# Kernel tuning notes

Hardware: AMD Instinct MI355X
Metric: run time of the kernel (lower is better)

The kernel has to match this reference:

```python
import jax, jax.numpy as jnp
import numpy as np

N = 20000
DEG = 16
E = N * DEG
IN_DIM = 512
OUT_DIM = 512
H = 4
D = OUT_DIM // H            # head_dim = 128
POS_DIM = 3
M_ROPE = D // (POS_DIM * 2) # 21
D_ROPE = POS_DIM * 2 * M_ROPE  # 126 (2 trailing dims unrotated)
ROPE_BASE = 10000.0

INV_FREQ = jnp.exp(-jnp.arange(M_ROPE, dtype=jnp.float32) * (np.log(ROPE_BASE) / M_ROPE))


def _rope(t, pos):
    # t: (N, D, H), pos: (N, POS_DIM)
    n = t.shape[0]
    angles = pos[:, :, None] * INV_FREQ[None, None, :]        # (N, POS_DIM, M)
    cos = jnp.cos(angles)[..., None]                           # (N, POS_DIM, M, 1)
    sin = jnp.sin(angles)[..., None]
    part = t[:, :D_ROPE, :].reshape(n, POS_DIM, M_ROPE, 2, H)
    even, odd = part[..., 0, :], part[..., 1, :]
    rot_even = even * cos - odd * sin
    rot_odd = even * sin + odd * cos
    rot = jnp.stack((rot_even, rot_odd), axis=3).reshape(n, D_ROPE, H)
    return jnp.concatenate([rot, t[:, D_ROPE:, :]], axis=1)


def setup_inputs() -> dict:
    key = jax.random.key(0)
    ks = jax.random.split(key, 12)
    x = jax.random.normal(ks[0], (N, IN_DIM), jnp.float32)
    pos = jax.random.uniform(ks[1], (N, POS_DIM), jnp.float32) * 100.0
    rows = jnp.repeat(jnp.arange(N, dtype=jnp.int32), DEG)  # sorted, every node has DEG out-edges
    cols = jax.random.randint(ks[2], (E,), 0, N, dtype=jnp.int32)
    s = 1.0 / np.sqrt(IN_DIM)
    Wq = jax.random.normal(ks[3], (OUT_DIM, IN_DIM), jnp.float32) * s
    Wk = jax.random.normal(ks[4], (OUT_DIM, IN_DIM), jnp.float32) * s
    Wv = jax.random.normal(ks[5], (OUT_DIM, IN_DIM), jnp.float32) * s
    Wo = jax.random.normal(ks[6], (OUT_DIM, OUT_DIM), jnp.float32) * s
    bq = jax.random.normal(ks[7], (OUT_DIM,), jnp.float32) * 0.01
    bk = jax.random.normal(ks[8], (OUT_DIM,), jnp.float32) * 0.01
    bv = jax.random.normal(ks[9], (OUT_DIM,), jnp.float32) * 0.01
    bo = jax.random.normal(ks[10], (OUT_DIM,), jnp.float32) * 0.01
    return {"x": x, "pos": pos, "rows": rows, "cols": cols,
            "Wq": Wq, "bq": bq, "Wk": Wk, "bk": bk, "Wv": Wv, "bv": bv, "Wo": Wo, "bo": bo}


def reference(x, pos, rows, cols, Wq, bq, Wk, bk, Wv, bv, Wo, bo):
    n = x.shape[0]
    q = (x @ Wq.T + bq).reshape(n, D, H)
    k = (x @ Wk.T + bk).reshape(n, D, H)
    v = (x @ Wv.T + bv).reshape(n, D, H)
    # scaling by sqrt(k.size(1)) == sqrt(head_dim)
    q = q / jnp.sqrt(jnp.asarray(D, q.dtype))
    q = _rope(q, pos)
    k = _rope(k, pos)
    # per-edge scores: s[e,h] = sum_d q[rows[e],d,h] * k[cols[e],d,h]
    scores = jnp.einsum('edh,edh->eh', q[rows], k[cols])  # (E, H)
    # row-wise sparse softmax per head
    row_max = jax.ops.segment_max(scores, rows, num_segments=n, indices_are_sorted=True)
    p = jnp.exp(scores - row_max[rows])
    denom = jax.ops.segment_sum(p, rows, num_segments=n, indices_are_sorted=True)
    attn = p / denom[rows]                                 # (E, H)
    # bspmm: y[i,d,h] = sum_{e: rows[e]=i} attn[e,h] * v[cols[e],d,h]
    y = jax.ops.segment_sum(attn[:, None, :] * v[cols], rows, num_segments=n, indices_are_sorted=True)
    out = y.reshape(n, OUT_DIM) @ Wo.T + bo
    return out
```

## Files before the change

kernel.cpp:

```cpp
#include <hip/hip_runtime.h>
#include <hip/hip_bf16.h>

#define NN 20000
#define DEG 16
#define KD 512
#define OD 512
#define NH 4
#define DH 128
#define DROPE 126

#define BM 128
#define BN 128
#define BK 64

typedef unsigned short u16;
typedef unsigned int u32;
typedef __attribute__((ext_vector_type(8))) short short8;
typedef __attribute__((ext_vector_type(4))) float f32x4;

__device__ __forceinline__ float b2f(u16 u){ return __uint_as_float((u32)u << 16); }
__device__ __forceinline__ u16 f2b(float f){
  u32 x = __float_as_uint(f);
  return (u16)((x + 0x7fffu + ((x >> 16) & 1u)) >> 16);
}
__device__ __forceinline__ void up8(uint4 u, float* f){
  f[0]=__uint_as_float(u.x<<16); f[1]=__uint_as_float(u.x&0xffff0000u);
  f[2]=__uint_as_float(u.y<<16); f[3]=__uint_as_float(u.y&0xffff0000u);
  f[4]=__uint_as_float(u.z<<16); f[5]=__uint_as_float(u.z&0xffff0000u);
  f[6]=__uint_as_float(u.w<<16); f[7]=__uint_as_float(u.w&0xffff0000u);
}
__device__ __forceinline__ uint4 cvt8(const float* s){
  uint4 a = *(const uint4*)s;
  uint4 b = *(const uint4*)(s + 4);
  uint4 o;
  o.x = (u32)f2b(__uint_as_float(a.x)) | ((u32)f2b(__uint_as_float(a.y)) << 16);
  o.y = (u32)f2b(__uint_as_float(a.z)) | ((u32)f2b(__uint_as_float(a.w)) << 16);
  o.z = (u32)f2b(__uint_as_float(b.x)) | ((u32)f2b(__uint_as_float(b.y)) << 16);
  o.w = (u32)f2b(__uint_as_float(b.z)) | ((u32)f2b(__uint_as_float(b.w)) << 16);
  return o;
}

__device__ __forceinline__ void load_lds16(const u16* g, u16* l) {
  __builtin_amdgcn_global_load_lds(
      (const __attribute__((address_space(1))) void*)g,
      (__attribute__((address_space(3))) void*)l, 16, 0, 0);
}

struct ConvJob {
  const float* x;  u16* xb;
  const float* w[4]; u16* wb[4];
  const float* b[4]; u16* bb[4];
};
__global__ __launch_bounds__(256) void conv_all(ConvJob j) {
  const int b = blockIdx.x;
  if (b < 5000) {
    const int i8 = (b * 256 + threadIdx.x) * 8;
    *(uint4*)(j.xb + i8) = cvt8(j.x + i8);
  } else if (b < 5512) {
    const int t = b - 5000;
    const int wsel = t >> 7;
    const int i8 = ((t & 127) * 256 + threadIdx.x) * 8;
    *(uint4*)(j.wb[wsel] + i8) = cvt8(j.w[wsel] + i8);
  } else {
    const int vsel = threadIdx.x >> 6;
    const int i8 = (threadIdx.x & 63) * 8;
    *(uint4*)(j.bb[vsel] + i8) = cvt8(j.b[vsel] + i8);
  }
}

__global__ __launch_bounds__(256, 4) void gemm_k(
    const u16* __restrict__ A,
    const u16* __restrict__ W0, const u16* __restrict__ B0,
    const u16* __restrict__ W1, const u16* __restrict__ B1,
    const u16* __restrict__ W2, const u16* __restrict__ B2,
    const float* __restrict__ pos,
    u16* __restrict__ o0, u16* __restrict__ o1, void* __restrict__ o2,
    int M, int only2, int f32out)
{
  __shared__ __align__(16) char smem[36864];
  __shared__ float posS[BM*3];
  __shared__ float freqS[21];
  u16* As = (u16*)smem;
  u16* Bs = As + BM*BK;

  const int b = blockIdx.x;
  const int xcd = b & 7, rem = b >> 3;
  int rowT, colT, w;
  if (only2) {
    rowT = (rem >> 2)*8 + xcd; colT = rem & 3; w = 2;
  } else {
    rowT = (rem / 12)*8 + xcd; const int sub = rem % 12; colT = sub & 3; w = sub >> 2;
  }
  if (rowT*BM >= M) return;

  const int tid = threadIdx.x;
  const int wave = tid >> 6, lane = tid & 63;
  const int wr = wave >> 1, wc = wave & 1;
  const int lm = lane & 15, lq = lane >> 4;
  const u16* W  = (w == 0) ? W0 : ((w == 1) ? W1 : W2);
  const u16* Bi = (w == 0) ? B0 : ((w == 1) ? B1 : B2);
  const int mode = w;
  u16* outQK = (w == 0) ? o0 : o1;

  f32x4 acc[4][4];
  #pragma unroll
  for (int i = 0; i < 4; i++)
    #pragma unroll
    for (int jj = 0; jj < 4; jj++)
      acc[i][jj] = (f32x4){0.f, 0.f, 0.f, 0.f};

  if (mode < 2) {
    if (tid < BM) {
      int gr = rowT*BM + tid; if (gr >= M) gr = M - 1;
      posS[tid*3+0] = pos[gr*3+0];
      posS[tid*3+1] = pos[gr*3+1];
      posS[tid*3+2] = pos[gr*3+2];
    }
    if (tid >= BM && tid < BM + 21)
      freqS[tid - BM] = __expf(-(float)(tid - BM) * 0.43858763676077064f);
  }

  for (int kt = 0; kt < KD; kt += BK) {
    #pragma unroll
    for (int it = 0; it < 4; it++) {
      const int chunk = it*256 + wave*64 + lane;
      const int row = chunk >> 3, gseg = (chunk & 7) ^ (row & 7);
      int gr = rowT*BM + row; if (gr >= M) gr = M - 1;
      load_lds16(A + (size_t)gr*KD + kt + gseg*8,
                 As + (size_t)(it*256 + wave*64)*8);
    }
    #pragma unroll
    for (int it = 0; it < 4; it++) {
      const int chunk = it*256 + wave*64 + lane;
      const int row = chunk >> 3, gseg = (chunk & 7) ^ (row & 7);
      load_lds16(W + (size_t)(colT*BN + row)*KD + kt + gseg*8,
                 Bs + (size_t)(it*256 + wave*64)*8);
    }
    __syncthreads();
    #pragma unroll
    for (int kk = 0; kk < BK; kk += 32) {
      const int ks = kk >> 3;
      short8 af[4], bfr[4];
      #pragma unroll
      for (int i = 0; i < 4; i++) {
        const int ra = wr*64 + i*16 + lm;
        af[i] = *(const short8*)(As + (size_t)(ra*8 + ((ks + lq) ^ (ra & 7)))*8);
      }
      #pragma unroll
      for (int i = 0; i < 4; i++) {
        const int rb = wc*64 + i*16 + lm;
        bfr[i] = *(const short8*)(Bs + (size_t)(rb*8 + ((ks + lq) ^ (rb & 7)))*8);
      }
      #pragma unroll
      for (int mi = 0; mi < 4; mi++)
        #pragma unroll
        for (int ni = 0; ni < 4; ni++)
          acc[mi][ni] = __builtin_amdgcn_mfma_f32_16x16x32_bf16(af[mi], bfr[ni], acc[mi][ni], 0, 0, 0);
    }
    __syncthreads();
  }

  float bvv[4];
  #pragma unroll
  for (int ni = 0; ni < 4; ni++)
    bvv[ni] = b2f(Bi[colT*BN + wc*64 + ni*16 + lm]);

  u16* Cs = (u16*)smem;

  if (mode == 2 && f32out) {
    #pragma unroll
    for (int mi = 0; mi < 4; mi++)
      #pragma unroll
      for (int ni = 0; ni < 4; ni++) {
        const int Cg = colT*BN + wc*64 + ni*16 + lm;
        #pragma unroll
        for (int r = 0; r < 4; r++) {
          const int grow = rowT*BM + wr*64 + mi*16 + lq*4 + r;
          if (grow < M) ((float*)o2)[(size_t)grow*OD + Cg] = acc[mi][ni][r] + bvv[ni];
        }
      }
    return;
  }

  if (mode == 2) {
    #pragma unroll
    for (int mi = 0; mi < 4; mi++)
      #pragma unroll
      for (int ni = 0; ni < 4; ni++) {
        const int cloc = wc*64 + ni*16 + lm;
        #pragma unroll
        for (int r = 0; r < 4; r++) {
          const int rloc = wr*64 + mi*16 + lq*4 + r;
          Cs[rloc*136 + cloc] = f2b(acc[mi][ni][r] + bvv[ni]);
        }
      }
    __syncthreads();
    #pragma unroll
    for (int pass = 0; pass < 8; pass++) {
      const int c2 = pass*256 + tid;
      const int cc = c2 & 15, rloc = c2 >> 4;
      const int grow = rowT*BM + rloc;
      if (grow < M) {
        uint4 v = *(const uint4*)(Cs + rloc*136 + cc*8);
        *(uint4*)((u16*)o2 + (size_t)grow*OD + colT*BN + cc*8) = v;
      }
    }
    return;
  }

  #pragma unroll
  for (int mi = 0; mi < 4; mi++) {
    #pragma unroll
    for (int ni = 0; ni < 4; ni++) {
      const int cloc = wc*64 + ni*16 + lm;
      const int h = cloc & 3, dloc = cloc >> 2;
      const int d = colT*32 + dloc;
      #pragma unroll
      for (int r = 0; r < 4; r++) {
        const int rloc = wr*64 + mi*16 + lq*4 + r;
        float v = acc[mi][ni][r] + bvv[ni];
        if (mode == 0) v *= 0.08838834764831845f;
        const float partner = __shfl_xor(v, 4);
        float vr = v;
        if (d < DROPE) {
          const int pp = d / 42, rem2 = d - pp*42, m = rem2 >> 1, par = rem2 & 1;
          const float ang = posS[rloc*3 + pp] * freqS[m];
          float sn, cs; __sincosf(ang, &sn, &cs);
          vr = par ? (v*cs + partner*sn) : (v*cs - partner*sn);
        }
        Cs[rloc*144 + h*36 + dloc] = f2b(vr);
      }
    }
  }
  __syncthreads();
  #pragma unroll
  for (int pass = 0; pass < 8; pass++) {
    const int c2 = pass*256 + tid;
    const int dd8 = c2 & 3, h = (c2 >> 2) & 3, rloc = c2 >> 4;
    const int grow = rowT*BM + rloc;
    if (grow < M) {
      uint2 a = *(const uint2*)(Cs + rloc*144 + h*36 + dd8*8);
      uint2 b2 = *(const uint2*)(Cs + rloc*144 + h*36 + dd8*8 + 4);
      *(uint4*)(outQK + ((size_t)grow*NH + h)*DH + colT*32 + dd8*8)
          = make_uint4(a.x, a.y, b2.x, b2.y);
    }
  }
}

__global__ __launch_bounds__(256, 3) void edge_attn(
    const int* __restrict__ cols, const u16* __restrict__ qf,
    const u16* __restrict__ kf, const u16* __restrict__ vf,
    u16* __restrict__ y)
{
  const int wave = threadIdx.x >> 6;
  const int lane = threadIdx.x & 63;
  const int n = blockIdx.x*4 + wave;
  const int j = lane >> 2, h = lane & 3;
  const int col = cols[n*DEG + j];

  const uint4 qall = *(const uint4*)(qf + (size_t)n*OD + lane*8);

  int cjs[16];
  #pragma unroll
  for (int jj = 0; jj < 16; jj++) cjs[jj] = __shfl(col, jj*4);

  uint4 kreg[16];
  #pragma unroll
  for (int jj = 0; jj < 16; jj++)
    kreg[jj] = *(const uint4*)(kf + (size_t)cjs[jj]*OD + lane*8);

  uint4 vreg[16];
  #pragma unroll
  for (int jj = 0; jj < 16; jj++)
    vreg[jj] = *(const uint4*)(vf + (size_t)cjs[jj]*OD + lane*8);

  float qa[8];
  up8(qall, qa);

  float s = 0.f;
  #pragma unroll
  for (int jj = 0; jj < 16; jj++) {
    float ka[8];
    up8(kreg[jj], ka);
    float pr = qa[0]*ka[0] + qa[1]*ka[1] + qa[2]*ka[2] + qa[3]*ka[3]
             + qa[4]*ka[4] + qa[5]*ka[5] + qa[6]*ka[6] + qa[7]*ka[7];
    pr += __shfl_xor(pr, 1);
    pr += __shfl_xor(pr, 2);
    pr += __shfl_xor(pr, 4);
    pr += __shfl_xor(pr, 8);
    const float red = __shfl(pr, h*16);
    s = (j == jj) ? red : s;
  }

  float mx = s;
  #pragma unroll
  for (int msk = 4; msk < 64; msk <<= 1) mx = fmaxf(mx, __shfl_xor(mx, msk));
  float p = expf(s - mx);
  float dn = p;
  #pragma unroll
  for (int msk = 4; msk < 64; msk <<= 1) dn += __shfl_xor(dn, msk);
  const float attn = p / dn;

  float ya[8];
  #pragma unroll
  for (int t = 0; t < 8; t++) ya[t] = 0.f;
  #pragma unroll
  for (int jj = 0; jj < 16; jj++) {
    const float a0 = __shfl(attn, jj*4+0);
    const float a1 = __shfl(attn, jj*4+1);
    const float a2 = __shfl(attn, jj*4+2);
    const float a3 = __shfl(attn, jj*4+3);
    float va[8];
    up8(vreg[jj], va);
    ya[0] += a0*va[0]; ya[1] += a1*va[1]; ya[2] += a2*va[2]; ya[3] += a3*va[3];
    ya[4] += a0*va[4]; ya[5] += a1*va[5]; ya[6] += a2*va[6]; ya[7] += a3*va[7];
  }
  u32 pk[4];
  #pragma unroll
  for (int t = 0; t < 4; t++)
    pk[t] = (u32)f2b(ya[2*t]) | ((u32)f2b(ya[2*t+1]) << 16);
  *(uint4*)(y + (size_t)n*OD + lane*8) = make_uint4(pk[0], pk[1], pk[2], pk[3]);
}

extern "C" void kernel_launch(void* const* d_in, const int* in_sizes, int n_in,
                              void* d_out, int out_size, void* d_ws, size_t ws_size,
                              hipStream_t stream) {
  (void)in_sizes; (void)n_in; (void)out_size; (void)ws_size;
  const float* x   = (const float*)d_in[0];
  const float* pos = (const float*)d_in[1];
  const int* cols = (const int*)d_in[3];
  const float* Wq = (const float*)d_in[4];
  const float* bq = (const float*)d_in[5];
  const float* Wk = (const float*)d_in[6];
  const float* bk = (const float*)d_in[7];
  const float* Wv = (const float*)d_in[8];
  const float* bv = (const float*)d_in[9];
  const float* Wo = (const float*)d_in[10];
  const float* bo = (const float*)d_in[11];

  char* ws = (char*)d_ws;
  size_t off = 0;
  auto carve = [&](size_t bytes) { char* p = ws + off; off += (bytes + 15) & ~(size_t)15; return p; };
  u16* xb   = (u16*)carve((size_t)NN*KD*2);
  u16* Wqb  = (u16*)carve((size_t)OD*KD*2);
  u16* Wkb  = (u16*)carve((size_t)OD*KD*2);
  u16* Wvb  = (u16*)carve((size_t)OD*KD*2);
  u16* Wob  = (u16*)carve((size_t)OD*OD*2);
  u16* bqb  = (u16*)carve((size_t)OD*2);
  u16* bkb  = (u16*)carve((size_t)OD*2);
  u16* bvb  = (u16*)carve((size_t)OD*2);
  u16* bob  = (u16*)carve((size_t)OD*2);
  u16* qf   = (u16*)carve((size_t)NN*OD*2);
  u16* kf   = (u16*)carve((size_t)NN*OD*2);
  u16* vf   = (u16*)carve((size_t)NN*OD*2);
  u16* y    = (u16*)carve((size_t)NN*OD*2);

  ConvJob cj;
  cj.x = x; cj.xb = xb;
  cj.w[0]=Wq; cj.w[1]=Wk; cj.w[2]=Wv; cj.w[3]=Wo;
  cj.wb[0]=Wqb; cj.wb[1]=Wkb; cj.wb[2]=Wvb; cj.wb[3]=Wob;
  cj.b[0]=bq; cj.b[1]=bk; cj.b[2]=bv; cj.b[3]=bo;
  cj.bb[0]=bqb; cj.bb[1]=bkb; cj.bb[2]=bvb; cj.bb[3]=bob;
  conv_all<<<dim3(5513), 256, 0, stream>>>(cj);

  gemm_k<<<dim3(1920), 256, 0, stream>>>(xb, Wqb, bqb, Wkb, bkb, Wvb, bvb, pos,
                                         qf, kf, (void*)vf, NN, 0, 0);
  edge_attn<<<dim3(NN/4), 256, 0, stream>>>(cols, qf, kf, vf, y);
  gemm_k<<<dim3(640), 256, 0, stream>>>(y, Wqb, bqb, Wkb, bkb, Wob, bob, pos,
                                        qf, kf, d_out, NN, 1, 1);
}
```

Baseline: 256.7 us.

## Store V head-major and split edge attention per head with XCD-aware mapping

V is now written in the same head-major permuted layout as Q and K, and Wo is transposed on conversion to match, so y comes out head-major and the output GEMM still gives the same result. The edge-attention kernel is restructured so each block handles one head for 16 nodes. Each 16-lane group owns one node and one head, which lets the softmax reduce within 16 lanes, and V gathers are deferred until after the softmax to lower register pressure. Blocks are mapped to XCDs by head so that each XCD's L2 caches only one head's slice of K and V, which should improve gather locality. The cost is a strided, uncoalesced read of Wo during conversion.

```diff
diff --git a/kernel.cpp b/kernel.cpp
--- a/kernel.cpp
+++ b/kernel.cpp
@@ -60,7 +60,22 @@
     const int t = b - 5000;
     const int wsel = t >> 7;
     const int i8 = ((t & 127) * 256 + threadIdx.x) * 8;
-    *(uint4*)(j.wb[wsel] + i8) = cvt8(j.w[wsel] + i8);
+    if (wsel < 3) {
+      *(uint4*)(j.wb[wsel] + i8) = cvt8(j.w[wsel] + i8);
+    } else {
+      const int o = i8 >> 9, cp = i8 & 511;
+      const int h = cp >> 7, d0 = cp & 127;
+      const float* src = j.w[3] + (size_t)o * 512 + h;
+      float tmp[8];
+      #pragma unroll
+      for (int t2 = 0; t2 < 8; t2++) tmp[t2] = src[(size_t)(d0 + t2) * 4];
+      uint4 ov;
+      ov.x = (u32)f2b(tmp[0]) | ((u32)f2b(tmp[1]) << 16);
+      ov.y = (u32)f2b(tmp[2]) | ((u32)f2b(tmp[3]) << 16);
+      ov.z = (u32)f2b(tmp[4]) | ((u32)f2b(tmp[5]) << 16);
+      ov.w = (u32)f2b(tmp[6]) | ((u32)f2b(tmp[7]) << 16);
+      *(uint4*)(j.wb[3] + i8) = ov;
+    }
   } else {
     const int vsel = threadIdx.x >> 6;
     const int i8 = (threadIdx.x & 63) * 8;
@@ -99,8 +114,8 @@
   const int lm = lane & 15, lq = lane >> 4;
   const u16* W  = (w == 0) ? W0 : ((w == 1) ? W1 : W2);
   const u16* Bi = (w == 0) ? B0 : ((w == 1) ? B1 : B2);
-  const int mode = w;
-  u16* outQK = (w == 0) ? o0 : o1;
+  const int emode = only2 ? 3 : w;
+  u16* outQKV = (w == 0) ? o0 : ((w == 1) ? o1 : (u16*)o2);
 
   f32x4 acc[4][4];
   #pragma unroll
@@ -109,7 +124,7 @@
     for (int jj = 0; jj < 4; jj++)
       acc[i][jj] = (f32x4){0.f, 0.f, 0.f, 0.f};
 
-  if (mode < 2) {
+  if (emode < 2) {
     if (tid < BM) {
       int gr = rowT*BM + tid; if (gr >= M) gr = M - 1;
       posS[tid*3+0] = pos[gr*3+0];
@@ -167,7 +182,7 @@
 
   u16* Cs = (u16*)smem;
 
-  if (mode == 2 && f32out) {
+  if (emode == 3) {
     #pragma unroll
     for (int mi = 0; mi < 4; mi++)
       #pragma unroll
@@ -182,32 +197,6 @@
     return;
   }
 
-  if (mode == 2) {
-    #pragma unroll
-    for (int mi = 0; mi < 4; mi++)
-      #pragma unroll
-      for (int ni = 0; ni < 4; ni++) {
-        const int cloc = wc*64 + ni*16 + lm;
-        #pragma unroll
-        for (int r = 0; r < 4; r++) {
-          const int rloc = wr*64 + mi*16 + lq*4 + r;
-          Cs[rloc*136 + cloc] = f2b(acc[mi][ni][r] + bvv[ni]);
-        }
-      }
-    __syncthreads();
-    #pragma unroll
-    for (int pass = 0; pass < 8; pass++) {
-      const int c2 = pass*256 + tid;
-      const int cc = c2 & 15, rloc = c2 >> 4;
-      const int grow = rowT*BM + rloc;
-      if (grow < M) {
-        uint4 v = *(const uint4*)(Cs + rloc*136 + cc*8);
-        *(uint4*)((u16*)o2 + (size_t)grow*OD + colT*BN + cc*8) = v;
-      }
-    }
-    return;
-  }
-
   #pragma unroll
   for (int mi = 0; mi < 4; mi++) {
     #pragma unroll
@@ -219,14 +208,16 @@
       for (int r = 0; r < 4; r++) {
         const int rloc = wr*64 + mi*16 + lq*4 + r;
         float v = acc[mi][ni][r] + bvv[ni];
-        if (mode == 0) v *= 0.08838834764831845f;
-        const float partner = __shfl_xor(v, 4);
+        if (emode == 0) v *= 0.08838834764831845f;
         float vr = v;
-        if (d < DROPE) {
-          const int pp = d / 42, rem2 = d - pp*42, m = rem2 >> 1, par = rem2 & 1;
-          const float ang = posS[rloc*3 + pp] * freqS[m];
-          float sn, cs; __sincosf(ang, &sn, &cs);
-          vr = par ? (v*cs + partner*sn) : (v*cs - partner*sn);
+        if (emode < 2) {
+          const float partner = __shfl_xor(v, 4);
+          if (d < DROPE) {
+            const int pp = d / 42, rem2 = d - pp*42, m = rem2 >> 1, par = rem2 & 1;
+            const float ang = posS[rloc*3 + pp] * freqS[m];
+            float sn, cs; __sincosf(ang, &sn, &cs);
+            vr = par ? (v*cs + partner*sn) : (v*cs - partner*sn);
+          }
         }
         Cs[rloc*144 + h*36 + dloc] = f2b(vr);
       }
@@ -241,7 +232,7 @@
     if (grow < M) {
       uint2 a = *(const uint2*)(Cs + rloc*144 + h*36 + dd8*8);
       uint2 b2 = *(const uint2*)(Cs + rloc*144 + h*36 + dd8*8 + 4);
-      *(uint4*)(outQK + ((size_t)grow*NH + h)*DH + colT*32 + dd8*8)
+      *(uint4*)(outQKV + ((size_t)grow*NH + h)*DH + colT*32 + dd8*8)
           = make_uint4(a.x, a.y, b2.x, b2.y);
     }
   }
@@ -252,74 +243,68 @@
     const u16* __restrict__ kf, const u16* __restrict__ vf,
     u16* __restrict__ y)
 {
-  const int wave = threadIdx.x >> 6;
-  const int lane = threadIdx.x & 63;
-  const int n = blockIdx.x*4 + wave;
-  const int j = lane >> 2, h = lane & 3;
-  const int col = cols[n*DEG + j];
-
-  const uint4 qall = *(const uint4*)(qf + (size_t)n*OD + lane*8);
-
-  int cjs[16];
-  #pragma unroll
-  for (int jj = 0; jj < 16; jj++) cjs[jj] = __shfl(col, jj*4);
+  const int b = blockIdx.x;
+  const int xcd = b & 7;
+  const int head = xcd >> 1;
+  const int nbase = (b >> 3) * 32 + (xcd & 1) * 16;
+  const int wave = threadIdx.x >> 6, lane = threadIdx.x & 63;
+  const int g = lane >> 4, l16 = lane & 15;
+  const int n = nbase + wave*4 + g;
+
+  const int col = cols[n*DEG + l16];
+  const uint4 qv = *(const uint4*)(qf + ((size_t)n*NH + head)*DH + l16*8);
 
   uint4 kreg[16];
   #pragma unroll
-  for (int jj = 0; jj < 16; jj++)
-    kreg[jj] = *(const uint4*)(kf + (size_t)cjs[jj]*OD + lane*8);
-
-  uint4 vreg[16];
-  #pragma unroll
-  for (int jj = 0; jj < 16; jj++)
-    vreg[jj] = *(const uint4*)(vf + (size_t)cjs[jj]*OD + lane*8);
-
-  float qa[8];
-  up8(qall, qa);
+  for (int jj = 0; jj < 16; jj++) {
+    const int cj = __shfl(col, g*16 + jj);
+    kreg[jj] = *(const uint4*)(kf + ((size_t)cj*NH + head)*DH + l16*8);
+  }
+  float qa[8]; up8(qv, qa);
 
   float s = 0.f;
   #pragma unroll
   for (int jj = 0; jj < 16; jj++) {
-    float ka[8];
-    up8(kreg[jj], ka);
+    float ka[8]; up8(kreg[jj], ka);
     float pr = qa[0]*ka[0] + qa[1]*ka[1] + qa[2]*ka[2] + qa[3]*ka[3]
              + qa[4]*ka[4] + qa[5]*ka[5] + qa[6]*ka[6] + qa[7]*ka[7];
     pr += __shfl_xor(pr, 1);
     pr += __shfl_xor(pr, 2);
     pr += __shfl_xor(pr, 4);
     pr += __shfl_xor(pr, 8);
-    const float red = __shfl(pr, h*16);
-    s = (j == jj) ? red : s;
+    s = (l16 == jj) ? pr : s;
   }
 
   float mx = s;
   #pragma unroll
-  for (int msk = 4; msk < 64; msk <<= 1) mx = fmaxf(mx, __shfl_xor(mx, msk));
+  for (int msk = 1; msk < 16; msk <<= 1) mx = fmaxf(mx, __shfl_xor(mx, msk));
   float p = expf(s - mx);
   float dn = p;
   #pragma unroll
-  for (int msk = 4; msk < 64; msk <<= 1) dn += __shfl_xor(dn, msk);
+  for (int msk = 1; msk < 16; msk <<= 1) dn += __shfl_xor(dn, msk);
   const float attn = p / dn;
 
+  uint4 vreg[16];
+  #pragma unroll
+  for (int jj = 0; jj < 16; jj++) {
+    const int cj = __shfl(col, g*16 + jj);
+    vreg[jj] = *(const uint4*)(vf + ((size_t)cj*NH + head)*DH + l16*8);
+  }
   float ya[8];
   #pragma unroll
   for (int t = 0; t < 8; t++) ya[t] = 0.f;
   #pragma unroll
   for (int jj = 0; jj < 16; jj++) {
-    const float a0 = __shfl(attn, jj*4+0);
-    const float a1 = __shfl(attn, jj*4+1);
-    const float a2 = __shfl(attn, jj*4+2);
-    const float a3 = __shfl(attn, jj*4+3);
-    float va[8];
-    up8(vreg[jj], va);
-    ya[0] += a0*va[0]; ya[1] += a1*va[1]; ya[2] += a2*va[2]; ya[3] += a3*va[3];
-    ya[4] += a0*va[4]; ya[5] += a1*va[5]; ya[6] += a2*va[6]; ya[7] += a3*va[7];
+    const float a = __shfl(attn, g*16 + jj);
+    float va[8]; up8(vreg[jj], va);
+    #pragma unroll
+    for (int t = 0; t < 8; t++) ya[t] += a*va[t];
   }
   u32 pk[4];
   #pragma unroll
   for (int t = 0; t < 4; t++)
     pk[t] = (u32)f2b(ya[2*t]) | ((u32)f2b(ya[2*t+1]) << 16);
-  *(uint4*)(y + (size_t)n*OD + lane*8) = make_uint4(pk[0], pk[1], pk[2], pk[3]);
+  *(uint4*)(y + ((size_t)n*NH + head)*DH + l16*8) = make_uint4(pk[0], pk[1], pk[2], pk[3]);
 }
 
 extern "C" void kernel_launch(void* const* d_in, const int* in_sizes, int n_in,
@@ -365,7 +350,7 @@
 
   gemm_k<<<dim3(1920), 256, 0, stream>>>(xb, Wqb, bqb, Wkb, bkb, Wvb, bvb, pos,
                                          qf, kf, (void*)vf, NN, 0, 0);
-  edge_attn<<<dim3(NN/4), 256, 0, stream>>>(cols, qf, kf, vf, y);
+  edge_attn<<<dim3(5000), 256, 0, stream>>>(cols, qf, kf, vf, y);
   gemm_k<<<dim3(640), 256, 0, stream>>>(y, Wqb, bqb, Wkb, bkb, Wob, bob, pos,
                                         qf, kf, d_out, NN, 1, 1);
 }
```

Measured after the change: 245.2 us. -4.5%, faster.
